# Kernel optimization log

Measured on AMD Instinct MI355X. Metric: run time of the kernel, lower is better.

## Reference

```python
import jax, jax.numpy as jnp
import numpy as np

N_NODES = 100000


def gcn_conv(x, src, dst, W, b, n_nodes):
    # PyG GCNConv: h = x @ W; add self-loops; symmetric norm; scatter-add; + bias
    h = x @ W  # [N, F_out]
    deg = jax.ops.segment_sum(jnp.ones_like(src, dtype=h.dtype), dst, num_segments=n_nodes)
    dinv = jnp.where(deg > 0, jax.lax.rsqrt(deg), 0.0)
    norm = dinv[src] * dinv[dst]  # [E+N]
    msgs = h[src] * norm[:, None]  # gather + scale
    out = jax.ops.segment_sum(msgs, dst, num_segments=n_nodes)  # scatter-add
    return out + b


def setup_inputs() -> dict:
    key = jax.random.key(0)
    ks = jax.random.split(key, 8)
    n, e, f_in, h = N_NODES, 1600000, 128, 64
    x = jax.random.normal(ks[0], (n, f_in), dtype=jnp.float32)
    edge_index = jax.random.randint(ks[1], (2, e), 0, n, dtype=jnp.int64)
    W1 = jax.random.normal(ks[2], (f_in, h), dtype=jnp.float32) / np.sqrt(f_in)
    b1 = jnp.zeros((h,), dtype=jnp.float32)
    W2 = jax.random.normal(ks[3], (h, h), dtype=jnp.float32) / np.sqrt(h)
    b2 = jnp.zeros((h,), dtype=jnp.float32)
    Wd = jax.random.normal(ks[4], (h, 1), dtype=jnp.float32) / np.sqrt(h)
    bd = jnp.zeros((1,), dtype=jnp.float32)
    return {"x": x, "edge_index": edge_index, "W1": W1, "b1": b1,
            "W2": W2, "b2": b2, "Wd": Wd, "bd": bd}


def reference(x, edge_index, W1, b1, W2, b2, Wd, bd):
    n = x.shape[0]
    loop = jnp.arange(n, dtype=edge_index.dtype)
    src = jnp.concatenate([edge_index[0], loop])  # add self-loops once
    dst = jnp.concatenate([edge_index[1], loop])
    h = jax.nn.relu(gcn_conv(x, src, dst, W1, b1, n))
    h = jax.nn.relu(gcn_conv(h, src, dst, W2, b2, n))
    return h @ Wd + bd
```

## Files before the change

### kernel.cpp

```cpp
#include <hip/hip_runtime.h>

#define NF 64
#define NBLK 256
#define SH 8
#define BMSK 255
#define MAXNB 2048

typedef unsigned short ushort_t;
typedef __attribute__((ext_vector_type(8))) short short8;
typedef __attribute__((ext_vector_type(4))) float f32x4;

__device__ inline ushort_t f2bf(float f) {
    unsigned u = __float_as_uint(f);
    return (ushort_t)((u + 0x7fffu + ((u >> 16) & 1u)) >> 16);
}
__device__ inline float bfhi(unsigned x) { return __uint_as_float(x & 0xffff0000u); }
__device__ inline float bflo(unsigned x) { return __uint_as_float(x << 16); }

#define PACK8(b, ua, ub) \
    b[0] = (short)f2bf(ua.x); b[1] = (short)f2bf(ua.y); \
    b[2] = (short)f2bf(ua.z); b[3] = (short)f2bf(ua.w); \
    b[4] = (short)f2bf(ub.x); b[5] = (short)f2bf(ub.y); \
    b[6] = (short)f2bf(ub.z); b[7] = (short)f2bf(ub.w);


__device__ inline int wave_incl_scan(int x, int lane) {
#pragma unroll
    for (int o = 1; o < 64; o <<= 1) { int y = __shfl_up(x, o, 64); if (lane >= o) x += y; }
    return x;
}

__global__ __launch_bounds__(256) void k_scan_a(const int* __restrict__ in, int* __restrict__ out,
                                                int* __restrict__ bsums, int n) {
    int t = threadIdx.x, lane = t & 63, wv = t >> 6;
    int base = blockIdx.x * 1024 + t * 4;
    int v[4]; int s = 0;
#pragma unroll
    for (int k = 0; k < 4; ++k) { int i = base + k; int x = (i < n) ? in[i] : 0; v[k] = s; s += x; }
    int incl = wave_incl_scan(s, lane);
    __shared__ int ws[4];
    if (lane == 63) ws[wv] = incl;
    __syncthreads();
    int wofs = 0;
#pragma unroll
    for (int w = 0; w < 4; ++w) if (w < wv) wofs += ws[w];
    int texcl = wofs + incl - s;
#pragma unroll
    for (int k = 0; k < 4; ++k) { int i = base + k; if (i < n) out[i] = texcl + v[k]; }
    if (t == 255) bsums[blockIdx.x] = wofs + incl;
}

__global__ __launch_bounds__(256) void k_scan_addb(int* __restrict__ data, const int* __restrict__ bsums,
                                                   int* __restrict__ bptr, int ntot, int E) {
    __shared__ int off_s;
    int t = threadIdx.x;
    int myChunk = (int)(blockIdx.x >> 2);
    if (t < 64) {
        int s = 0;
        for (int i = t; i < myChunk; i += 64) s += bsums[i];
#pragma unroll
        for (int o = 32; o > 0; o >>= 1) s += __shfl_xor(s, o, 64);
        if (t == 0) off_s = s;
    }
    __syncthreads();
    int off = off_s;
    int i = blockIdx.x * 256 + t;
    if (i < ntot) {
        int v = data[i] + off;
        data[i] = v;
        if ((i & (NBLK - 1)) == 0) bptr[i / NBLK] = v;
    }
    if (i == 0) bptr[ntot / NBLK] = E;
}


__global__ __launch_bounds__(256) void k_histA(const int* __restrict__ dst, int* __restrict__ hmat,
                                               int E, int NB, int chunk,
                                               const float* __restrict__ W1, const float* __restrict__ W2,
                                               ushort_t* __restrict__ w1f, ushort_t* __restrict__ w2f) {
    __shared__ int h[MAXNB];
    int blk = blockIdx.x;
    int gid = blk * 256 + threadIdx.x;
    if (gid < 8192) {
        int k = gid >> 6, c = gid & 63;
        int f = ((k >> 5) << 2) | (c >> 4);
        int ln = (c & 15) | (((k >> 3) & 3) << 4);
        w1f[f * 512 + ln * 8 + (k & 7)] = f2bf(W1[gid]);
    } else if (gid < 12288) {
        int i2 = gid - 8192;
        int k = i2 >> 6, c = i2 & 63;
        int f = ((k >> 5) << 2) | (c >> 4);
        int ln = (c & 15) | (((k >> 3) & 3) << 4);
        w2f[f * 512 + ln * 8 + (k & 7)] = f2bf(W2[i2]);
    }

    for (int i = threadIdx.x; i < NB; i += 256) h[i] = 0;
    __syncthreads();
    int beg = blk * chunk, end = beg + chunk; if (end > E) end = E;
    for (int e = beg + threadIdx.x; e < end; e += 256) atomicAdd(&h[dst[e] >> SH], 1);
    __syncthreads();
    for (int i = threadIdx.x; i < NB; i += 256) hmat[i * NBLK + blk] = h[i];
}

__global__ __launch_bounds__(256) void k_placeB(const int* __restrict__ src, const int* __restrict__ dst,
                                                const int* __restrict__ hmat, int* __restrict__ pairs,
                                                int E, int NB, int chunk) {
    __shared__ int cur[MAXNB];
    int blk = blockIdx.x;
    for (int i = threadIdx.x; i < NB; i += 256) cur[i] = hmat[i * NBLK + blk];
    __syncthreads();
    int beg = blk * chunk, end = beg + chunk; if (end > E) end = E;
    for (int e = beg + threadIdx.x; e < end; e += 256) {
        int s = src[e], d = dst[e];
        int off = atomicAdd(&cur[d >> SH], 1);
        pairs[off] = (s << SH) | (d & BMSK);
    }
}

__global__ __launch_bounds__(256) void k_csr(const int* __restrict__ bptr, const int* __restrict__ pairs,
                                             int* __restrict__ row_ptr, int* __restrict__ cnt,
                                             float* __restrict__ dinv, int* __restrict__ col, int n) {
    __shared__ int h[256];
    __shared__ int cur[256];
    __shared__ int ws[4];
    int b = blockIdx.x, t = threadIdx.x;
    h[t] = 0;
    __syncthreads();
    int beg = bptr[b], end = bptr[b + 1];
    for (int j = beg + t; j < end; j += 256) atomicAdd(&h[pairs[j] & BMSK], 1);
    __syncthreads();
    int c = h[t];
    int incl = wave_incl_scan(c, t & 63);
    if ((t & 63) == 63) ws[t >> 6] = incl;
    __syncthreads();
    int wofs = 0;
#pragma unroll
    for (int w = 0; w < 4; ++w) if (w < (t >> 6)) wofs += ws[w];
    int ex = wofs + incl - c;
    int node = (b << SH) + t;
    if (node < n) {
        row_ptr[node] = beg + ex;
        cnt[node] = c;
        dinv[node] = rsqrtf(1.0f + (float)c);
    }
    cur[t] = beg + ex;
    __syncthreads();
    for (int j = beg + t; j < end; j += 256) {
        int pk = pairs[j];
        int p = atomicAdd(&cur[pk & BMSK], 1);
        col[p] = pk >> SH;
    }
}

__global__ __launch_bounds__(256) void k_mm1(
    const float* __restrict__ X, const ushort_t* __restrict__ w1f,
    const float* __restrict__ dinv, ushort_t* __restrict__ out, int n)
{
    int t = threadIdx.x;
    int lane = t & 63, wv = t >> 6;
    int r16 = lane & 15, kg = lane >> 4;

    short8 a0[4], a1[4], a2[4], a3[4];
#pragma unroll
    for (int f = 0; f < 4; ++f) {
        a0[f] = *(const short8*)(w1f + (0 + f) * 512 + lane * 8);
        a1[f] = *(const short8*)(w1f + (4 + f) * 512 + lane * 8);
        a2[f] = *(const short8*)(w1f + (8 + f) * 512 + lane * 8);
        a3[f] = *(const short8*)(w1f + (12 + f) * 512 + lane * 8);
    }

    int tile = blockIdx.x * 4 + wv;
    int row = tile * 16 + r16;
    int r = (row < n) ? row : (n - 1);
    const float* pX = X + (size_t)r * 128 + kg * 8;

    float4 u0a = *(const float4*)(pX + 0),   u0b = *(const float4*)(pX + 4);
    float4 u1a = *(const float4*)(pX + 32),  u1b = *(const float4*)(pX + 36);
    float4 u2a = *(const float4*)(pX + 64),  u2b = *(const float4*)(pX + 68);
    float4 u3a = *(const float4*)(pX + 96),  u3b = *(const float4*)(pX + 100);

    short8 b0, b1, b2, b3;
    PACK8(b0, u0a, u0b); PACK8(b1, u1a, u1b);
    PACK8(b2, u2a, u2b); PACK8(b3, u3a, u3b);

    f32x4 z = {0.f, 0.f, 0.f, 0.f};
    f32x4 acc[4];
#pragma unroll
    for (int f = 0; f < 4; ++f)
        acc[f] = __builtin_amdgcn_mfma_f32_16x16x32_bf16(a0[f], b0, z, 0, 0, 0);
#pragma unroll
    for (int f = 0; f < 4; ++f)
        acc[f] = __builtin_amdgcn_mfma_f32_16x16x32_bf16(a1[f], b1, acc[f], 0, 0, 0);
#pragma unroll
    for (int f = 0; f < 4; ++f)
        acc[f] = __builtin_amdgcn_mfma_f32_16x16x32_bf16(a2[f], b2, acc[f], 0, 0, 0);
#pragma unroll
    for (int f = 0; f < 4; ++f)
        acc[f] = __builtin_amdgcn_mfma_f32_16x16x32_bf16(a3[f], b3, acc[f], 0, 0, 0);

    if (row < n) {
        float di = dinv[row];
#pragma unroll
        for (int f = 0; f < 4; ++f) {
            ushort4 o;
            o.x = f2bf(acc[f][0] * di); o.y = f2bf(acc[f][1] * di);
            o.z = f2bf(acc[f][2] * di); o.w = f2bf(acc[f][3] * di);
            *(ushort4*)(out + (size_t)row * NF + f * 16 + kg * 4) = o;
        }
    }
}

__global__ __launch_bounds__(256) void k_pullmm(
    const ushort_t* __restrict__ hs, const float* __restrict__ dinv,
    const int* __restrict__ row_ptr, const int* __restrict__ cnt,
    const int* __restrict__ col, const float* __restrict__ bias,
    const ushort_t* __restrict__ w2f, ushort_t* __restrict__ out, int n)
{
    __shared__ ushort_t bfrag[1024];
    int t = threadIdx.x;
    int lane = t & 63, wv = t >> 6;

    short8 aflo = *(const short8*)(w2f + wv * 512 + lane * 8);
    short8 afhi = *(const short8*)(w2f + (4 + wv) * 512 + lane * 8);

    int d = blockIdx.x * 16 + (t >> 4);
    int lt = t & 15;
    int fo = lt << 2;
    int grpbase = t & 48;
    const char* __restrict__ hp = (const char*)hs;
    unsigned lt8 = (unsigned)lt << 3;
    float rx = 0.f, ry = 0.f, rz = 0.f, rw = 0.f;
    if (d < n) {
        uint2 sv = *(const uint2*)(hp + (((unsigned)d << 7) + lt8));
        float4 acc = make_float4(bflo(sv.x), bfhi(sv.x), bflo(sv.y), bfhi(sv.y));
        int beg = row_ptr[d], deg = cnt[d];
        for (int jb = 0; jb < deg; jb += 16) {
            int m = deg - jb; if (m > 16) m = 16;
            int idx = (lt < m) ? col[beg + jb + lt] : 0;
            uint2 v[16];
#pragma unroll
            for (int u = 0; u < 16; ++u) {
                int kk = (u < m) ? u : (m - 1);
                int s = __shfl(idx, grpbase + kk, 64);
                v[u] = *(const uint2*)(hp + (((unsigned)s << 7) + lt8));
            }
#pragma unroll
            for (int u = 0; u < 16; ++u) {
                if (u < m) {
                    acc.x += bflo(v[u].x); acc.y += bfhi(v[u].x);
                    acc.z += bflo(v[u].y); acc.w += bfhi(v[u].y);
                }
            }
        }
        float di = dinv[d];
        float4 bv = *(const float4*)(bias + fo);
        rx = fmaxf(fmaf(acc.x, di, bv.x), 0.0f);
        ry = fmaxf(fmaf(acc.y, di, bv.y), 0.0f);
        rz = fmaxf(fmaf(acc.z, di, bv.z), 0.0f);
        rw = fmaxf(fmaf(acc.w, di, bv.w), 0.0f);
    }
    {
        ushort4 o;
        o.x = f2bf(rx); o.y = f2bf(ry); o.z = f2bf(rz); o.w = f2bf(rw);
        int g = t >> 4;
        int ks = lt >> 3, kg2 = (lt >> 1) & 3, half = lt & 1;
        *(ushort4*)(bfrag + ks * 512 + (((kg2 << 4) | g) << 3) + (half << 2)) = o;
    }
    __syncthreads();

    int r16 = lane & 15, kg = lane >> 4;
    short8 bb0 = *(const short8*)(bfrag + lane * 8);
    short8 bb1 = *(const short8*)(bfrag + 512 + lane * 8);

    f32x4 z = {0.f, 0.f, 0.f, 0.f};
    f32x4 acc2 = __builtin_amdgcn_mfma_f32_16x16x32_bf16(aflo, bb0, z, 0, 0, 0);
    acc2 = __builtin_amdgcn_mfma_f32_16x16x32_bf16(afhi, bb1, acc2, 0, 0, 0);

    int row = blockIdx.x * 16 + r16;
    if (row < n) {
        float di = dinv[row];
        ushort4 o;
        o.x = f2bf(acc2[0] * di); o.y = f2bf(acc2[1] * di);
        o.z = f2bf(acc2[2] * di); o.w = f2bf(acc2[3] * di);
        *(ushort4*)((char*)out + (((unsigned)row << 7) + ((unsigned)wv << 5) + ((unsigned)kg << 3))) = o;
    }
}

__global__ __launch_bounds__(256) void k_pull2(
    const ushort_t* __restrict__ hs, const float* __restrict__ dinv,
    const int* __restrict__ row_ptr, const int* __restrict__ cnt,
    const int* __restrict__ col, const float* __restrict__ bias,
    const float* __restrict__ Wd, const float* __restrict__ bd,
    float* __restrict__ outv, int n)
{
    int d = blockIdx.x * 16 + (threadIdx.x >> 4);
    if (d >= n) return;
    int lt = threadIdx.x & 15;
    int fo = lt << 2;
    int grpbase = threadIdx.x & 48;
    const char* __restrict__ hp = (const char*)hs;
    unsigned lt8 = (unsigned)lt << 3;
    int beg = row_ptr[d], deg = cnt[d];

    uint2 sv = *(const uint2*)(hp + (((unsigned)d << 7) + lt8));
    float4 acc = make_float4(bflo(sv.x), bfhi(sv.x), bflo(sv.y), bfhi(sv.y));

    for (int jb = 0; jb < deg; jb += 16) {
        int m = deg - jb; if (m > 16) m = 16;
        int idx = (lt < m) ? col[beg + jb + lt] : 0;
        uint2 v[16];
#pragma unroll
        for (int u = 0; u < 16; ++u) {
            int kk = (u < m) ? u : (m - 1);
            int s = __shfl(idx, grpbase + kk, 64);
            v[u] = *(const uint2*)(hp + (((unsigned)s << 7) + lt8));
        }
#pragma unroll
        for (int u = 0; u < 16; ++u) {
            if (u < m) {
                acc.x += bflo(v[u].x); acc.y += bfhi(v[u].x);
                acc.z += bflo(v[u].y); acc.w += bfhi(v[u].y);
            }
        }
    }

    float di = dinv[d];
    float4 bv = *(const float4*)(bias + fo);
    float rx = fmaxf(fmaf(acc.x, di, bv.x), 0.0f);
    float ry = fmaxf(fmaf(acc.y, di, bv.y), 0.0f);
    float rz = fmaxf(fmaf(acc.z, di, bv.z), 0.0f);
    float rw = fmaxf(fmaf(acc.w, di, bv.w), 0.0f);

    float4 wv = *(const float4*)(Wd + fo);
    float vsum = rx * wv.x + ry * wv.y + rz * wv.z + rw * wv.w;
#pragma unroll
    for (int o = 1; o < 16; o <<= 1) vsum += __shfl_xor(vsum, o, 64);
    if (lt == 0) outv[d] = vsum + bd[0];
}

extern "C" void kernel_launch(void* const* d_in, const int* in_sizes, int n_in,
                              void* d_out, int out_size, void* d_ws, size_t ws_size,
                              hipStream_t stream) {
    const float* x  = (const float*)d_in[0];
    const int*   ei = (const int*)d_in[1];
    const float* W1 = (const float*)d_in[2];
    const float* b1 = (const float*)d_in[3];
    const float* W2 = (const float*)d_in[4];
    const float* b2 = (const float*)d_in[5];
    const float* Wd = (const float*)d_in[6];
    const float* bd = (const float*)d_in[7];
    float* out = (float*)d_out;

    int n = in_sizes[0] / 128;
    int E = in_sizes[1] / 2;
    const int* src = ei;
    const int* dst = ei + E;

    int NB = (n + (1 << SH) - 1) >> SH;
    int chunk = (E + NBLK - 1) / NBLK;
    int ntot = NB * NBLK;
    int nsb = (ntot + 1023) / 1024;
    int ntiles = (n + 15) / 16;

    float* dinv    = (float*)d_ws;
    float* bufH    = dinv + n;
    float* bufA    = bufH + (size_t)n * NF;
    int*   counts  = (int*)(bufA + (size_t)n * NF);
    int*   row_ptr = counts + n;
    int*   col     = row_ptr + n;
    int*   hmat    = col + E;
    int*   bptr    = hmat + ntot;
    int*   bsums   = bptr + NB + 1;
    int*   wfrags  = bsums + 2048;
    ushort_t* w1f  = (ushort_t*)wfrags;
    ushort_t* w2f  = w1f + 8192;
    int*   pairs   = (int*)bufH;
    ushort_t* hsb  = (ushort_t*)bufH;
    ushort_t* hs2b = (ushort_t*)bufA;

    k_histA<<<NBLK, 256, 0, stream>>>(dst, hmat, E, NB, chunk, W1, W2, w1f, w2f);
    k_scan_a<<<nsb, 256, 0, stream>>>(hmat, hmat, bsums, ntot);
    k_scan_addb<<<(ntot + 255) / 256, 256, 0, stream>>>(hmat, bsums, bptr, ntot, E);
    k_placeB<<<NBLK, 256, 0, stream>>>(src, dst, hmat, pairs, E, NB, chunk);

    k_csr<<<NB, 256, 0, stream>>>(bptr, pairs, row_ptr, counts, dinv, col, n);

    k_mm1<<<(ntiles + 3) / 4, 256, 0, stream>>>(x, w1f, dinv, hsb, n);

    k_pullmm<<<(n + 15) / 16, 256, 0, stream>>>(hsb, dinv, row_ptr, counts, col, b1,
                                                w2f, hs2b, n);

    k_pull2<<<(n + 15) / 16, 256, 0, stream>>>(hs2b, dinv, row_ptr, counts, col, b2,
                                               Wd, bd, out, n);
}
```

Baseline: 126.6 us.

## Fuse CSR build with first-layer matmul into a single kernel

Merges the per-bucket CSR construction kernel with the X@W1 MFMA kernel, so each 256-node block computes degrees, writes the CSR columns, then multiplies its own 256 rows using the dinv values it keeps in shared memory. This removes one kernel launch and the global reload of dinv. The pairs buffer moves into the upper half of bufA because hsb (aliasing bufH) is now written in the same kernel that reads pairs. Only NB (~391) blocks now run the matmul, each covering 16 tiles, which lowers parallelism compared with the old one-tile-per-wave grid.

Result: no change. 124.3 us (-1.8%).

```diff
diff --git a/kernel.cpp b/kernel.cpp
--- a/kernel.cpp
+++ b/kernel.cpp
@@ -117,11 +117,16 @@
     }
 }
 
-__global__ __launch_bounds__(256) void k_csr(const int* __restrict__ bptr, const int* __restrict__ pairs,
-                                             int* __restrict__ row_ptr, int* __restrict__ cnt,
-                                             float* __restrict__ dinv, int* __restrict__ col, int n) {
+__global__ __launch_bounds__(256) void k_csrmm(
+    const int* __restrict__ bptr, const int* __restrict__ pairs,
+    int* __restrict__ row_ptr, int* __restrict__ cnt,
+    float* __restrict__ dinv, int* __restrict__ col,
+    const float* __restrict__ X, const ushort_t* __restrict__ w1f,
+    ushort_t* __restrict__ hsb, int n)
+{
     __shared__ int h[256];
     __shared__ int cur[256];
+    __shared__ float ds[256];
     __shared__ int ws[4];
     int b = blockIdx.x, t = threadIdx.x;
     h[t] = 0;
@@ -137,26 +142,24 @@
 #pragma unroll
     for (int w = 0; w < 4; ++w) if (w < (t >> 6)) wofs += ws[w];
     int ex = wofs + incl - c;
-    int node = (b << SH) + t;
+    int node0 = b << SH;
+    int node = node0 + t;
+    float di_t = rsqrtf(1.0f + (float)c);
     if (node < n) {
         row_ptr[node] = beg + ex;
         cnt[node] = c;
-        dinv[node] = rsqrtf(1.0f + (float)c);
+        dinv[node] = di_t;
     }
     cur[t] = beg + ex;
-    __syncthreads();
+    ds[t] = di_t;
+    __syncthreads();
+
     for (int j = beg + t; j < end; j += 256) {
         int pk = pairs[j];
         int p = atomicAdd(&cur[pk & BMSK], 1);
         col[p] = pk >> SH;
     }
-}
-
-__global__ __launch_bounds__(256) void k_mm1(
-    const float* __restrict__ X, const ushort_t* __restrict__ w1f,
-    const float* __restrict__ dinv, ushort_t* __restrict__ out, int n)
-{
-    int t = threadIdx.x;
+
     int lane = t & 63, wv = t >> 6;
     int r16 = lane & 15, kg = lane >> 4;
 
@@ -169,43 +172,45 @@
         a3[f] = *(const short8*)(w1f + (12 + f) * 512 + lane * 8);
     }
 
-    int tile = blockIdx.x * 4 + wv;
-    int row = tile * 16 + r16;
-    int r = (row < n) ? row : (n - 1);
-    const float* pX = X + (size_t)r * 128 + kg * 8;
-
-    float4 u0a = *(const float4*)(pX + 0),   u0b = *(const float4*)(pX + 4);
-    float4 u1a = *(const float4*)(pX + 32),  u1b = *(const float4*)(pX + 36);
-    float4 u2a = *(const float4*)(pX + 64),  u2b = *(const float4*)(pX + 68);
-    float4 u3a = *(const float4*)(pX + 96),  u3b = *(const float4*)(pX + 100);
-
-    short8 b0, b1, b2, b3;
-    PACK8(b0, u0a, u0b); PACK8(b1, u1a, u1b);
-    PACK8(b2, u2a, u2b); PACK8(b3, u3a, u3b);
-
-    f32x4 z = {0.f, 0.f, 0.f, 0.f};
-    f32x4 acc[4];
-#pragma unroll
-    for (int f = 0; f < 4; ++f)
-        acc[f] = __builtin_amdgcn_mfma_f32_16x16x32_bf16(a0[f], b0, z, 0, 0, 0);
-#pragma unroll
-    for (int f = 0; f < 4; ++f)
-        acc[f] = __builtin_amdgcn_mfma_f32_16x16x32_bf16(a1[f], b1, acc[f], 0, 0, 0);
-#pragma unroll
-    for (int f = 0; f < 4; ++f)
-        acc[f] = __builtin_amdgcn_mfma_f32_16x16x32_bf16(a2[f], b2, acc[f], 0, 0, 0);
-#pragma unroll
-    for (int f = 0; f < 4; ++f)
-        acc[f] = __builtin_amdgcn_mfma_f32_16x16x32_bf16(a3[f], b3, acc[f], 0, 0, 0);
-
-    if (row < n) {
-        float di = dinv[row];
-#pragma unroll
-        for (int f = 0; f < 4; ++f) {
-            ushort4 o;
-            o.x = f2bf(acc[f][0] * di); o.y = f2bf(acc[f][1] * di);
-            o.z = f2bf(acc[f][2] * di); o.w = f2bf(acc[f][3] * di);
-            *(ushort4*)(out + (size_t)row * NF + f * 16 + kg * 4) = o;
+    for (int tile = wv; tile < 16; tile += 4) {
+        int lrow = tile * 16 + r16;
+        int row = node0 + lrow;
+        int r = (row < n) ? row : (n - 1);
+        const float* pX = X + (size_t)r * 128 + kg * 8;
+
+        float4 u0a = *(const float4*)(pX + 0),   u0b = *(const float4*)(pX + 4);
+        float4 u1a = *(const float4*)(pX + 32),  u1b = *(const float4*)(pX + 36);
+        float4 u2a = *(const float4*)(pX + 64),  u2b = *(const float4*)(pX + 68);
+        float4 u3a = *(const float4*)(pX + 96),  u3b = *(const float4*)(pX + 100);
+
+        short8 b0, b1, b2, b3;
+        PACK8(b0, u0a, u0b); PACK8(b1, u1a, u1b);
+        PACK8(b2, u2a, u2b); PACK8(b3, u3a, u3b);
+
+        f32x4 z = {0.f, 0.f, 0.f, 0.f};
+        f32x4 acc[4];
+#pragma unroll
+        for (int f = 0; f < 4; ++f)
+            acc[f] = __builtin_amdgcn_mfma_f32_16x16x32_bf16(a0[f], b0, z, 0, 0, 0);
+#pragma unroll
+        for (int f = 0; f < 4; ++f)
+            acc[f] = __builtin_amdgcn_mfma_f32_16x16x32_bf16(a1[f], b1, acc[f], 0, 0, 0);
+#pragma unroll
+        for (int f = 0; f < 4; ++f)
+            acc[f] = __builtin_amdgcn_mfma_f32_16x16x32_bf16(a2[f], b2, acc[f], 0, 0, 0);
+#pragma unroll
+        for (int f = 0; f < 4; ++f)
+            acc[f] = __builtin_amdgcn_mfma_f32_16x16x32_bf16(a3[f], b3, acc[f], 0, 0, 0);
+
+        if (row < n) {
+            float di = ds[lrow];
+#pragma unroll
+            for (int f = 0; f < 4; ++f) {
+                ushort4 o;
+                o.x = f2bf(acc[f][0] * di); o.y = f2bf(acc[f][1] * di);
+                o.z = f2bf(acc[f][2] * di); o.w = f2bf(acc[f][3] * di);
+                *(ushort4*)(hsb + (size_t)row * NF + f * 16 + kg * 4) = o;
+            }
         }
     }
 }
@@ -360,7 +365,6 @@
     int chunk = (E + NBLK - 1) / NBLK;
     int ntot = NB * NBLK;
     int nsb = (ntot + 1023) / 1024;
-    int ntiles = (n + 15) / 16;
 
     float* dinv    = (float*)d_ws;
     float* bufH    = dinv + n;
@@ -374,18 +378,17 @@
     int*   wfrags  = bsums + 2048;
     ushort_t* w1f  = (ushort_t*)wfrags;
     ushort_t* w2f  = w1f + 8192;
-    int*   pairs   = (int*)bufH;
     ushort_t* hsb  = (ushort_t*)bufH;
     ushort_t* hs2b = (ushort_t*)bufA;
+    int*   pairs   = (int*)(bufA + (size_t)n * 32);
 
     k_histA<<<NBLK, 256, 0, stream>>>(dst, hmat, E, NB, chunk, W1, W2, w1f, w2f);
     k_scan_a<<<nsb, 256, 0, stream>>>(hmat, hmat, bsums, ntot);
     k_scan_addb<<<(ntot + 255) / 256, 256, 0, stream>>>(hmat, bsums, bptr, ntot, E);
     k_placeB<<<NBLK, 256, 0, stream>>>(src, dst, hmat, pairs, E, NB, chunk);
 
-    k_csr<<<NB, 256, 0, stream>>>(bptr, pairs, row_ptr, counts, dinv, col, n);
-
-    k_mm1<<<(ntiles + 3) / 4, 256, 0, stream>>>(x, w1f, dinv, hsb, n);
+    k_csrmm<<<NB, 256, 0, stream>>>(bptr, pairs, row_ptr, counts, dinv, col,
+                                    x, w1f, hsb, n);
 
     k_pullmm<<<(n + 15) / 16, 256, 0, stream>>>(hsb, dinv, row_ptr, counts, col, b1,
                                                 w2f, hs2b, n);
```
